# Performance work log

Measured on AMD Instinct MI355X. Metric: run time of the kernel, lower is better.

## Reference

```python
import jax, jax.numpy as jnp
import numpy as np

S = 160                 # image size (renderer default is 256; reduced for working-set budget)
SIGMA = 1.0             # soft-silhouette sharpness, in pixels
EPS = 1e-8
CHUNK = 512             # faces per rasterization chunk
ANGLE = np.pi / 2.0
VIEW_TAN = float(np.tan(np.radians(30.0)))   # nr.Renderer default viewing_angle=30
CAM_POS = np.array([0.0, 0.0, 2.732], dtype=np.float32)

# constant rotation: Rodrigues formula for axis-angle (pi/2 about y), as in nr.rotation_from_axis
_aa = ANGLE * np.array([0.0, 1.0, 0.0])
_th = np.linalg.norm(_aa)
_k = _aa / _th
_K = np.array([[0, -_k[2], _k[1]], [_k[2], 0, -_k[0]], [-_k[1], _k[0], 0]])
ROT = (np.eye(3) + np.sin(_th) * _K + (1 - np.cos(_th)) * (_K @ _K)).astype(np.float32)


def _make_uv_sphere(stacks=32, slices=64):
    verts = [[0.0, 0.0, 1.0]]
    for i in range(1, stacks):
        phi = np.pi * i / stacks
        for j in range(slices):
            th = 2 * np.pi * j / slices
            verts.append([np.sin(phi) * np.cos(th), np.sin(phi) * np.sin(th), np.cos(phi)])
    verts.append([0.0, 0.0, -1.0])
    V = len(verts)
    faces = []
    for j in range(slices):
        faces.append([0, 1 + j, 1 + (j + 1) % slices])
    for i in range(stacks - 2):
        r0 = 1 + i * slices
        r1 = r0 + slices
        for j in range(slices):
            a, b = r0 + j, r0 + (j + 1) % slices
            c, d = r1 + j, r1 + (j + 1) % slices
            faces.append([a, b, c])
            faces.append([b, d, c])
    r0 = 1 + (stacks - 2) * slices
    for j in range(slices):
        faces.append([V - 1, r0 + (j + 1) % slices, r0 + j])
    return np.asarray(verts, np.float32), np.asarray(faces, np.int32)


def setup_inputs() -> dict:
    key = jax.random.key(0)
    v, f = _make_uv_sphere()                     # V=1986, F=3968
    pad = 4096 - f.shape[0]
    f = np.concatenate([f, np.zeros((pad, 3), np.int32)], axis=0)  # degenerate pad faces
    image_ref = jax.random.uniform(key, (1, S, S), dtype=jnp.float32)
    return {"vertices": jnp.asarray(v)[None], "faces": jnp.asarray(f)[None], "image_ref": image_ref}


def _project(v):
    # world -> camera (rotate, place camera at z=2.732) -> perspective -> pixel coords
    vc = v @ ROT.T + CAM_POS                     # [V,3]
    xy = vc[:, :2] / (vc[:, 2:3] * VIEW_TAN)     # NDC in [-1,1]
    return (xy + 1.0) * (S / 2.0)                # [V,2] pixels


def _soft_coverage(pts, fv):
    # pts [P,2] pixel centers, fv [C,3,2] screen-space triangles -> coverage [P,C]
    a, b, c = fv[:, 0], fv[:, 1], fv[:, 2]

    def edge_dist(p0, p1):
        d = p1 - p0                                              # [C,2]
        cr = d[:, 0] * (pts[:, None, 1] - p0[None, :, 1]) - d[:, 1] * (pts[:, None, 0] - p0[None, :, 0])
        return cr / (jnp.sqrt(jnp.sum(d * d, -1)) + EPS)         # signed pixel distance [P,C]

    area = (b[:, 0] - a[:, 0]) * (c[:, 1] - a[:, 1]) - (b[:, 1] - a[:, 1]) * (c[:, 0] - a[:, 0])
    sg = jnp.where(area >= 0, 1.0, -1.0)[None, :]                # winding correction
    dmin = jnp.minimum(jnp.minimum(edge_dist(a, b) * sg, edge_dist(b, c) * sg), edge_dist(c, a) * sg)
    cov = jax.nn.sigmoid(dmin / SIGMA)
    return cov * (jnp.abs(area) > 1e-6)[None, :]                 # mask degenerate (padded) faces


def reference(vertices, faces, image_ref):
    v2 = _project(vertices[0])                   # [V,2]
    fv = v2[faces[0]]                            # [F,3,2]
    fvc = fv.reshape(-1, CHUNK, 3, 2)            # [F/CHUNK, CHUNK, 3, 2]
    ys, xs = jnp.meshgrid(jnp.arange(S, dtype=jnp.float32) + 0.5,
                          jnp.arange(S, dtype=jnp.float32) + 0.5, indexing="ij")
    pts = jnp.stack([xs.ravel(), ys.ravel()], -1)  # [P,2]

    cov_fn = jax.checkpoint(_soft_coverage)

    def body(not_cov, fvk):
        cov = cov_fn(pts, fvk)                   # [P,CHUNK]
        return not_cov * jnp.prod(1.0 - cov, axis=1), None

    not_cov, _ = jax.lax.scan(body, jnp.ones((S * S,), jnp.float32), fvc)
    images = (1.0 - not_cov).reshape(1, S, S)    # silhouette in [0,1]
    loss = jnp.sum((images - image_ref) ** 2)    # broadcast matches images - image_ref[None] in torch
    return images, loss
```

## Files before the change

kernel.cpp:

```cpp
#include <hip/hip_runtime.h>
#include <math.h>

#define S_IMG 160
#define NPIX (S_IMG * S_IMG)
#define NF 4096
#define NV 1986
#define TS 16
#define NTX 10
#define NTILE 100
#define CAP NF
#define SPLIT 16
#define INV_LN2 1.4426950408889634f
#define CULL_THRESH -25.0f

#define ROT_EPS 6.123234e-17f
#define CAM_Z 2.732f
#define VIEW_TAN 0.5773502691896258f

#if __has_builtin(__builtin_amdgcn_exp2f)
#define EXP2F(x) __builtin_amdgcn_exp2f(x)
#else
#define EXP2F(x) exp2f(x)
#endif

__global__ void __launch_bounds__(512) setup_cull(const float* __restrict__ verts,
                                                  const int* __restrict__ faces,
                                                  float* __restrict__ list,
                                                  int* __restrict__ nk_arr) {
    __shared__ float2 sverts[NV];
    __shared__ int wcnt[8];

    const int t = blockIdx.x;
    const int tid = threadIdx.x;
    const int wid = tid >> 6;
    const int lane = tid & 63;

    for (int i = tid; i < NV; i += 512) {
        float x = verts[3 * i], y = verts[3 * i + 1], z = verts[3 * i + 2];
        float vx = fmaf(ROT_EPS, x, z);
        float vz = fmaf(ROT_EPS, z, -x) + CAM_Z;
        float inv = __builtin_amdgcn_rcpf(vz * VIEW_TAN);
        sverts[i] = make_float2(fmaf(vx * inv, 80.0f, 80.0f),
                                fmaf(y * inv, 80.0f, 80.0f));
    }
    __syncthreads();

    const float cx = (float)((t % NTX) * TS) + 8.0f;
    const float cy = (float)((t / NTX) * TS) + 8.0f;
    float* mylist = list + (size_t)t * CAP * 12;
    int base = 0;

    for (int r = 0; r < NF / 512; ++r) {
        int f = r * 512 + tid;
        int i0 = faces[3 * f], i1 = faces[3 * f + 1], i2 = faces[3 * f + 2];
        float2 a = sverts[i0];
        float2 b = sverts[i1];
        float2 c = sverts[i2];
        float area = (b.x - a.x) * (c.y - a.y) - (b.y - a.y) * (c.x - a.x);
        float sg = (area >= 0.0f) ? INV_LN2 : -INV_LN2;
        bool valid = fabsf(area) > 1e-6f;

        float o[9];
        float umin = 1e30f;
        float2 p0s[3] = {a, b, c};
        float2 p1s[3] = {b, c, a};
#pragma unroll
        for (int e = 0; e < 3; ++e) {
            float dx = p1s[e].x - p0s[e].x;
            float dy = p1s[e].y - p0s[e].y;
            float dd = fmaf(dx, dx, dy * dy);
            float s = sg * __builtin_amdgcn_rsqf(dd);
            float A = valid ? (-dy * s) : 0.0f;
            float B = valid ? (dx * s) : 0.0f;
            float C = valid ? ((dy * p0s[e].x - dx * p0s[e].y) * s) : -1e30f;
            o[3 * e + 0] = A;
            o[3 * e + 1] = B;
            o[3 * e + 2] = C;
            float bound = fmaf(fabsf(A) + fabsf(B), 7.5f, fmaf(A, cx, fmaf(B, cy, C)));
            umin = fminf(umin, valid ? bound : -1e30f);
        }
        bool pred = umin >= CULL_THRESH;
        unsigned long long m = __ballot(pred);
        int wpop = __popcll(m);
        int prefix = __popcll(m & ((1ull << lane) - 1ull));

        __syncthreads();
        if (lane == 0) wcnt[wid] = wpop;
        __syncthreads();
        int off = base;
#pragma unroll
        for (int w = 0; w < 8; ++w) {
            int cw = wcnt[w];
            if (w < wid) off += cw;
            base += cw;
        }
        off += prefix;
        if (pred) {
            float4* dst = (float4*)(mylist + (size_t)off * 12);
            dst[0] = make_float4(o[0], o[1], o[2], o[3]);
            dst[1] = make_float4(o[4], o[5], o[6], o[7]);
            dst[2] = make_float4(o[8], 0.0f, 0.0f, 0.0f);
        }
    }
    __syncthreads();

    const int cnt = base;
    const int nkt = (cnt + 63) >> 6;
    int padcnt = nkt * 64 - cnt;
    for (int i = tid; i < padcnt; i += 512) {
        float4* dst = (float4*)(mylist + (size_t)(cnt + i) * 12);
        dst[0] = make_float4(0.0f, 0.0f, -64.0f, 0.0f);
        dst[1] = make_float4(0.0f, -64.0f, 0.0f, 0.0f);
        dst[2] = make_float4(-64.0f, 0.0f, 0.0f, 0.0f);
    }
    if (tid == 0) nk_arr[t] = nkt;
}

__global__ void __launch_bounds__(64) cover(const float* __restrict__ list,
                                            const int* __restrict__ nk_arr,
                                            float* __restrict__ pacc) {
    const int t = blockIdx.x;
    const int s = blockIdx.y;
    const int nkt = nk_arr[t];
    if (s >= nkt) return;

    const int lane = threadIdx.x;
    const int colL = lane & 15;
    const int rowL = (lane >> 4) * 4;
    const float px = (float)((t % NTX) * TS + colL) + 0.5f;
    const float py0 = (float)((t / NTX) * TS + rowL) + 0.5f;
    const float py1 = py0 + 1.0f, py2 = py0 + 2.0f, py3 = py0 + 3.0f;

    float P0 = 1.0f, P1 = 1.0f, P2 = 1.0f, P3 = 1.0f;

    for (int k = s; k < nkt; k += SPLIT) {
        const float* fptr = list + ((size_t)t * CAP + (size_t)k * 64) * 12;
#pragma unroll 4
        for (int j = 0; j < 64; ++j) {
            float4 c0 = *(const float4*)(fptr + 12 * j);
            float4 c1 = *(const float4*)(fptr + 12 * j + 4);
            float4 c2 = *(const float4*)(fptr + 12 * j + 8);
            float b1 = fmaf(c0.x, px, c0.z);
            float b2 = fmaf(c0.w, px, c1.y);
            float b3 = fmaf(c1.z, px, c2.x);
            {
                float d1 = fmaf(c0.y, py0, b1), d2 = fmaf(c1.x, py0, b2), d3 = fmaf(c1.w, py0, b3);
                float e = EXP2F(fminf(fminf(d1, d2), d3));
                P0 = fmaf(P0, e, P0);
            }
            {
                float d1 = fmaf(c0.y, py1, b1), d2 = fmaf(c1.x, py1, b2), d3 = fmaf(c1.w, py1, b3);
                float e = EXP2F(fminf(fminf(d1, d2), d3));
                P1 = fmaf(P1, e, P1);
            }
            {
                float d1 = fmaf(c0.y, py2, b1), d2 = fmaf(c1.x, py2, b2), d3 = fmaf(c1.w, py2, b3);
                float e = EXP2F(fminf(fminf(d1, d2), d3));
                P2 = fmaf(P2, e, P2);
            }
            {
                float d1 = fmaf(c0.y, py3, b1), d2 = fmaf(c1.x, py3, b2), d3 = fmaf(c1.w, py3, b3);
                float e = EXP2F(fminf(fminf(d1, d2), d3));
                P3 = fmaf(P3, e, P3);
            }
        }
    }

    size_t base = ((size_t)t * SPLIT + s) * 256 + (size_t)rowL * 16 + colL;
    pacc[base] = __builtin_amdgcn_rcpf(P0);
    pacc[base + 16] = __builtin_amdgcn_rcpf(P1);
    pacc[base + 32] = __builtin_amdgcn_rcpf(P2);
    pacc[base + 48] = __builtin_amdgcn_rcpf(P3);
}

__global__ void __launch_bounds__(256) finish(const float* __restrict__ pacc,
                                              const int* __restrict__ nk_arr,
                                              const float* __restrict__ img_ref,
                                              float* __restrict__ out,
                                              float* __restrict__ bsums) {
    const int t = blockIdx.x;
    const int tid = threadIdx.x;
    const int ns = min(nk_arr[t], SPLIT);
    float prod = 1.0f;
    for (int sI = 0; sI < ns; ++sI) prod *= pacc[((size_t)t * SPLIT + sI) * 256 + tid];
    float img = 1.0f - prod;
    int col = (t % NTX) * TS + (tid & 15);
    int row = (t / NTX) * TS + (tid >> 4);
    int p = row * S_IMG + col;
    out[p] = img;
    float d = img - img_ref[p];
    float sq = d * d;
#pragma unroll
    for (int off = 32; off > 0; off >>= 1) sq += __shfl_down(sq, off);
    __shared__ float red[4];
    int lane = tid & 63;
    int wid = tid >> 6;
    if (lane == 0) red[wid] = sq;
    __syncthreads();
    if (tid == 0) bsums[t] = (red[0] + red[1]) + (red[2] + red[3]);
}

__global__ void __launch_bounds__(64) loss_kernel(const float* __restrict__ bsums,
                                                  float* __restrict__ loss_out) {
    int lane = threadIdx.x;
    float v = 0.0f;
    if (lane < NTILE) v = bsums[lane];
    if (lane + 64 < NTILE) v += bsums[lane + 64];
#pragma unroll
    for (int off = 32; off > 0; off >>= 1) v += __shfl_down(v, off);
    if (lane == 0) loss_out[0] = v;
}

extern "C" void kernel_launch(void* const* d_in, const int* in_sizes, int n_in,
                              void* d_out, int out_size, void* d_ws, size_t ws_size,
                              hipStream_t stream) {
    const float* verts = (const float*)d_in[0];
    const int* faces = (const int*)d_in[1];
    const float* img_ref = (const float*)d_in[2];
    float* out = (float*)d_out;

    float* list = (float*)d_ws;
    float* pacc = list + (size_t)NTILE * CAP * 12;
    int* nk_arr = (int*)(pacc + (size_t)NTILE * SPLIT * 256);
    float* bsums = (float*)(nk_arr + 128);

    setup_cull<<<NTILE, 512, 0, stream>>>(verts, faces, list, nk_arr);
    cover<<<dim3(NTILE, SPLIT), 64, 0, stream>>>(list, nk_arr, pacc);
    finish<<<NTILE, 256, 0, stream>>>(pacc, nk_arr, img_ref, out, bsums);
    loss_kernel<<<1, 64, 0, stream>>>(bsums, out + NPIX);
}
```

Measured before the change: 39.35 us.

## Flatten tile×chunk work into a compacted item list with LDS-staged face data

```diff
diff --git a/kernel.cpp b/kernel.cpp
--- a/kernel.cpp
+++ b/kernel.cpp
@@ -9,7 +9,8 @@
 #define NTX 10
 #define NTILE 100
 #define CAP NF
-#define SPLIT 16
+#define MAXK 64
+#define NBLK 512
 #define INV_LN2 1.4426950408889634f
 #define CULL_THRESH -25.0f
 
@@ -116,30 +117,55 @@
     if (tid == 0) nk_arr[t] = nkt;
 }
 
-__global__ void __launch_bounds__(64) cover(const float* __restrict__ list,
-                                            const int* __restrict__ nk_arr,
-                                            float* __restrict__ pacc) {
-    const int t = blockIdx.x;
-    const int s = blockIdx.y;
-    const int nkt = nk_arr[t];
-    if (s >= nkt) return;
-
-    const int lane = threadIdx.x;
-    const int colL = lane & 15;
-    const int rowL = (lane >> 4) * 4;
-    const float px = (float)((t % NTX) * TS + colL) + 0.5f;
-    const float py0 = (float)((t / NTX) * TS + rowL) + 0.5f;
-    const float py1 = py0 + 1.0f, py2 = py0 + 2.0f, py3 = py0 + 3.0f;
-
-    float P0 = 1.0f, P1 = 1.0f, P2 = 1.0f, P3 = 1.0f;
-
-    for (int k = s; k < nkt; k += SPLIT) {
-        const float* fptr = list + ((size_t)t * CAP + (size_t)k * 64) * 12;
-#pragma unroll 4
+__global__ void __launch_bounds__(128) build_items(const int* __restrict__ nk_arr,
+                                                   int* __restrict__ cumk,
+                                                   int* __restrict__ items) {
+    __shared__ int scum[NTILE + 1];
+    if (threadIdx.x == 0) {
+        int acc = 0;
+        for (int t = 0; t < NTILE; ++t) { scum[t] = acc; acc += nk_arr[t]; }
+        scum[NTILE] = acc;
+        cumk[NTILE] = acc;
+    }
+    __syncthreads();
+    for (int t = threadIdx.x; t < NTILE; t += 128) {
+        int b = scum[t], n = scum[t + 1] - b;
+        cumk[t] = b;
+        for (int k = 0; k < n; ++k) items[b + k] = (t << 8) | k;
+    }
+}
+
+__global__ void __launch_bounds__(256) cover(const float* __restrict__ list,
+                                             const int* __restrict__ cumk,
+                                             const int* __restrict__ items,
+                                             float* __restrict__ partials) {
+    __shared__ float4 slot[4][64 * 3];
+    const int wid = threadIdx.x >> 6;
+    const int lane = threadIdx.x & 63;
+    const int NIT = cumk[NTILE];
+    const int NW = NBLK * 4;
+    float4* myslot = slot[wid];
+
+    for (int p = blockIdx.x * 4 + wid; p < NIT; p += NW) {
+        int item = items[p];
+        int t = item >> 8, k = item & 255;
+
+        const float4* src = (const float4*)(list + ((size_t)t * CAP + (size_t)k * 64) * 12);
+#pragma unroll
+        for (int i = 0; i < 3; ++i) myslot[lane + i * 64] = src[lane + i * 64];
+        asm volatile("s_waitcnt lgkmcnt(0)" ::: "memory");
+
+        const int colL = lane & 15;
+        const int rowL = (lane >> 4) * 4;
+        const float px = (float)((t % NTX) * TS + colL) + 0.5f;
+        const float py0 = (float)((t / NTX) * TS + rowL) + 0.5f;
+        const float py1 = py0 + 1.0f, py2 = py0 + 2.0f, py3 = py0 + 3.0f;
+
+        float P0 = 1.0f, P1 = 1.0f, P2 = 1.0f, P3 = 1.0f;
         for (int j = 0; j < 64; ++j) {
-            float4 c0 = *(const float4*)(fptr + 12 * j);
-            float4 c1 = *(const float4*)(fptr + 12 * j + 4);
-            float4 c2 = *(const float4*)(fptr + 12 * j + 8);
+            float4 c0 = myslot[3 * j];
+            float4 c1 = myslot[3 * j + 1];
+            float4 c2 = myslot[3 * j + 2];
             float b1 = fmaf(c0.x, px, c0.z);
             float b2 = fmaf(c0.w, px, c1.y);
             float b3 = fmaf(c1.z, px, c2.x);
@@ -164,25 +190,26 @@
                 P3 = fmaf(P3, e, P3);
             }
         }
-    }
-
-    size_t base = ((size_t)t * SPLIT + s) * 256 + (size_t)rowL * 16 + colL;
-    pacc[base] = __builtin_amdgcn_rcpf(P0);
-    pacc[base + 16] = __builtin_amdgcn_rcpf(P1);
-    pacc[base + 32] = __builtin_amdgcn_rcpf(P2);
-    pacc[base + 48] = __builtin_amdgcn_rcpf(P3);
-}
-
-__global__ void __launch_bounds__(256) finish(const float* __restrict__ pacc,
+        asm volatile("" ::: "memory");
+
+        size_t base = ((size_t)t * MAXK + k) * 256 + (size_t)rowL * 16 + colL;
+        partials[base] = __builtin_amdgcn_rcpf(P0);
+        partials[base + 16] = __builtin_amdgcn_rcpf(P1);
+        partials[base + 32] = __builtin_amdgcn_rcpf(P2);
+        partials[base + 48] = __builtin_amdgcn_rcpf(P3);
+    }
+}
+
+__global__ void __launch_bounds__(256) finish(const float* __restrict__ partials,
                                               const int* __restrict__ nk_arr,
                                               const float* __restrict__ img_ref,
                                               float* __restrict__ out,
                                               float* __restrict__ bsums) {
     const int t = blockIdx.x;
     const int tid = threadIdx.x;
-    const int ns = min(nk_arr[t], SPLIT);
+    const int nkt = nk_arr[t];
     float prod = 1.0f;
-    for (int sI = 0; sI < ns; ++sI) prod *= pacc[((size_t)t * SPLIT + sI) * 256 + tid];
+    for (int k = 0; k < nkt; ++k) prod *= partials[((size_t)t * MAXK + k) * 256 + tid];
     float img = 1.0f - prod;
     int col = (t % NTX) * TS + (tid & 15);
     int row = (t / NTX) * TS + (tid >> 4);
@@ -220,12 +247,15 @@
     float* out = (float*)d_out;
 
     float* list = (float*)d_ws;
-    float* pacc = list + (size_t)NTILE * CAP * 12;
-    int* nk_arr = (int*)(pacc + (size_t)NTILE * SPLIT * 256);
-    float* bsums = (float*)(nk_arr + 128);
+    float* partials = list + (size_t)NTILE * CAP * 12;
+    int* nk_arr = (int*)(partials + (size_t)NTILE * MAXK * 256);
+    int* cumk = nk_arr + 128;
+    int* items = cumk + 128;
+    float* bsums = (float*)(items + NTILE * MAXK + 128);
 
     setup_cull<<<NTILE, 512, 0, stream>>>(verts, faces, list, nk_arr);
-    cover<<<dim3(NTILE, SPLIT), 64, 0, stream>>>(list, nk_arr, pacc);
-    finish<<<NTILE, 256, 0, stream>>>(pacc, nk_arr, img_ref, out, bsums);
+    build_items<<<1, 128, 0, stream>>>(nk_arr, cumk, items);
+    cover<<<NBLK, 256, 0, stream>>>(list, cumk, items, partials);
+    finish<<<NTILE, 256, 0, stream>>>(partials, nk_arr, img_ref, out, bsums);
     loss_kernel<<<1, 64, 0, stream>>>(bsums, out + NPIX);
 }
```

Result: no change. 38.73 us (-1.6%).

## Use 16x32 tiles, one wave per face chunk with LDS-staged coefficients

Applied to the files above, without the earlier changes.

```diff
diff --git a/kernel.cpp b/kernel.cpp
--- a/kernel.cpp
+++ b/kernel.cpp
@@ -5,11 +5,11 @@
 #define NPIX (S_IMG * S_IMG)
 #define NF 4096
 #define NV 1986
-#define TS 16
-#define NTX 10
-#define NTILE 100
+#define NTTX 10
+#define NTILE2 50
 #define CAP NF
-#define SPLIT 16
+#define MAXK 64
+#define NBLK3 800
 #define INV_LN2 1.4426950408889634f
 #define CULL_THRESH -25.0f
 
@@ -23,19 +23,20 @@
 #define EXP2F(x) exp2f(x)
 #endif
 
-__global__ void __launch_bounds__(512) setup_cull(const float* __restrict__ verts,
-                                                  const int* __restrict__ faces,
-                                                  float* __restrict__ list,
-                                                  int* __restrict__ nk_arr) {
+__global__ void __launch_bounds__(1024) setup_cull(const float* __restrict__ verts,
+                                                   const int* __restrict__ faces,
+                                                   float4* __restrict__ qlist,
+                                                   float* __restrict__ c3list,
+                                                   int* __restrict__ nk_arr) {
     __shared__ float2 sverts[NV];
-    __shared__ int wcnt[8];
+    __shared__ int wcnt[16];
 
     const int t = blockIdx.x;
     const int tid = threadIdx.x;
     const int wid = tid >> 6;
     const int lane = tid & 63;
 
-    for (int i = tid; i < NV; i += 512) {
+    for (int i = tid; i < NV; i += 1024) {
         float x = verts[3 * i], y = verts[3 * i + 1], z = verts[3 * i + 2];
         float vx = fmaf(ROT_EPS, x, z);
         float vz = fmaf(ROT_EPS, z, -x) + CAM_Z;
@@ -45,13 +46,14 @@
     }
     __syncthreads();
 
-    const float cx = (float)((t % NTX) * TS) + 8.0f;
-    const float cy = (float)((t / NTX) * TS) + 8.0f;
-    float* mylist = list + (size_t)t * CAP * 12;
+    const float cx = (float)((t % NTTX) * 16) + 8.0f;
+    const float cy = (float)((t / NTTX) * 32) + 16.0f;
+    float4* myq = qlist + (size_t)t * CAP * 2;
+    float* myc = c3list + (size_t)t * CAP;
     int base = 0;
 
-    for (int r = 0; r < NF / 512; ++r) {
-        int f = r * 512 + tid;
+    for (int r = 0; r < NF / 1024; ++r) {
+        int f = r * 1024 + tid;
         int i0 = faces[3 * f], i1 = faces[3 * f + 1], i2 = faces[3 * f + 2];
         float2 a = sverts[i0];
         float2 b = sverts[i1];
@@ -76,7 +78,8 @@
             o[3 * e + 0] = A;
             o[3 * e + 1] = B;
             o[3 * e + 2] = C;
-            float bound = fmaf(fabsf(A) + fabsf(B), 7.5f, fmaf(A, cx, fmaf(B, cy, C)));
+            float bound = fmaf(fabsf(A), 7.5f,
+                         fmaf(fabsf(B), 15.5f, fmaf(A, cx, fmaf(B, cy, C))));
             umin = fminf(umin, valid ? bound : -1e30f);
         }
         bool pred = umin >= CULL_THRESH;
@@ -89,17 +92,16 @@
         __syncthreads();
         int off = base;
 #pragma unroll
-        for (int w = 0; w < 8; ++w) {
+        for (int w = 0; w < 16; ++w) {
             int cw = wcnt[w];
             if (w < wid) off += cw;
             base += cw;
         }
         off += prefix;
         if (pred) {
-            float4* dst = (float4*)(mylist + (size_t)off * 12);
-            dst[0] = make_float4(o[0], o[1], o[2], o[3]);
-            dst[1] = make_float4(o[4], o[5], o[6], o[7]);
-            dst[2] = make_float4(o[8], 0.0f, 0.0f, 0.0f);
+            myq[(size_t)off * 2] = make_float4(o[0], o[1], o[2], o[3]);
+            myq[(size_t)off * 2 + 1] = make_float4(o[4], o[5], o[6], o[7]);
+            myc[off] = o[8];
         }
     }
     __syncthreads();
@@ -107,105 +109,111 @@
     const int cnt = base;
     const int nkt = (cnt + 63) >> 6;
     int padcnt = nkt * 64 - cnt;
-    for (int i = tid; i < padcnt; i += 512) {
-        float4* dst = (float4*)(mylist + (size_t)(cnt + i) * 12);
-        dst[0] = make_float4(0.0f, 0.0f, -64.0f, 0.0f);
-        dst[1] = make_float4(0.0f, -64.0f, 0.0f, 0.0f);
-        dst[2] = make_float4(-64.0f, 0.0f, 0.0f, 0.0f);
+    for (int i = tid; i < padcnt; i += 1024) {
+        myq[(size_t)(cnt + i) * 2] = make_float4(0.0f, 0.0f, -64.0f, 0.0f);
+        myq[(size_t)(cnt + i) * 2 + 1] = make_float4(0.0f, -64.0f, 0.0f, 0.0f);
+        myc[cnt + i] = -64.0f;
     }
     if (tid == 0) nk_arr[t] = nkt;
 }
 
-__global__ void __launch_bounds__(64) cover(const float* __restrict__ list,
-                                            const int* __restrict__ nk_arr,
-                                            float* __restrict__ pacc) {
-    const int t = blockIdx.x;
-    const int s = blockIdx.y;
-    const int nkt = nk_arr[t];
-    if (s >= nkt) return;
-
-    const int lane = threadIdx.x;
+__global__ void __launch_bounds__(256) cover(const float4* __restrict__ qlist,
+                                             const float* __restrict__ c3list,
+                                             const int* __restrict__ nk_arr,
+                                             float* __restrict__ partials) {
+    __shared__ float4 sq[4][128];
+    __shared__ float sc[4][64];
+    const int wid = threadIdx.x >> 6;
+    const int lane = threadIdx.x & 63;
+    const int p = blockIdx.x * 4 + wid;
+    const int t = p >> 6;
+    const int k = p & 63;
+    if (k >= nk_arr[t]) return;
+
+    {
+        const float4* srcq = qlist + ((size_t)t * CAP + (size_t)k * 64) * 2;
+        const float* srcc = c3list + (size_t)t * CAP + (size_t)k * 64;
+        sq[wid][lane * 2] = srcq[lane * 2];
+        sq[wid][lane * 2 + 1] = srcq[lane * 2 + 1];
+        sc[wid][lane] = srcc[lane];
+    }
+    asm volatile("s_waitcnt lgkmcnt(0)" ::: "memory");
+
     const int colL = lane & 15;
-    const int rowL = (lane >> 4) * 4;
-    const float px = (float)((t % NTX) * TS + colL) + 0.5f;
-    const float py0 = (float)((t / NTX) * TS + rowL) + 0.5f;
-    const float py1 = py0 + 1.0f, py2 = py0 + 2.0f, py3 = py0 + 3.0f;
+    const int rowB = (lane >> 4) * 8;
+    const float px = (float)((t % NTTX) * 16 + colL) + 0.5f;
+    const float py0 = (float)((t / NTTX) * 32 + rowB) + 0.5f;
 
     float P0 = 1.0f, P1 = 1.0f, P2 = 1.0f, P3 = 1.0f;
-
-    for (int k = s; k < nkt; k += SPLIT) {
-        const float* fptr = list + ((size_t)t * CAP + (size_t)k * 64) * 12;
-#pragma unroll 4
-        for (int j = 0; j < 64; ++j) {
-            float4 c0 = *(const float4*)(fptr + 12 * j);
-            float4 c1 = *(const float4*)(fptr + 12 * j + 4);
-            float4 c2 = *(const float4*)(fptr + 12 * j + 8);
-            float b1 = fmaf(c0.x, px, c0.z);
-            float b2 = fmaf(c0.w, px, c1.y);
-            float b3 = fmaf(c1.z, px, c2.x);
-            {
-                float d1 = fmaf(c0.y, py0, b1), d2 = fmaf(c1.x, py0, b2), d3 = fmaf(c1.w, py0, b3);
-                float e = EXP2F(fminf(fminf(d1, d2), d3));
-                P0 = fmaf(P0, e, P0);
-            }
-            {
-                float d1 = fmaf(c0.y, py1, b1), d2 = fmaf(c1.x, py1, b2), d3 = fmaf(c1.w, py1, b3);
-                float e = EXP2F(fminf(fminf(d1, d2), d3));
-                P1 = fmaf(P1, e, P1);
-            }
-            {
-                float d1 = fmaf(c0.y, py2, b1), d2 = fmaf(c1.x, py2, b2), d3 = fmaf(c1.w, py2, b3);
-                float e = EXP2F(fminf(fminf(d1, d2), d3));
-                P2 = fmaf(P2, e, P2);
-            }
-            {
-                float d1 = fmaf(c0.y, py3, b1), d2 = fmaf(c1.x, py3, b2), d3 = fmaf(c1.w, py3, b3);
-                float e = EXP2F(fminf(fminf(d1, d2), d3));
-                P3 = fmaf(P3, e, P3);
-            }
-        }
-    }
-
-    size_t base = ((size_t)t * SPLIT + s) * 256 + (size_t)rowL * 16 + colL;
-    pacc[base] = __builtin_amdgcn_rcpf(P0);
-    pacc[base + 16] = __builtin_amdgcn_rcpf(P1);
-    pacc[base + 32] = __builtin_amdgcn_rcpf(P2);
-    pacc[base + 48] = __builtin_amdgcn_rcpf(P3);
-}
-
-__global__ void __launch_bounds__(256) finish(const float* __restrict__ pacc,
+    float P4 = 1.0f, P5 = 1.0f, P6 = 1.0f, P7 = 1.0f;
+
+    for (int j = 0; j < 64; ++j) {
+        float4 q0 = sq[wid][2 * j];
+        float4 q1 = sq[wid][2 * j + 1];
+        float c3 = sc[wid][j];
+        float b1 = fmaf(q0.x, px, q0.z);
+        float b2 = fmaf(q0.w, px, q1.y);
+        float b3 = fmaf(q1.z, px, c3);
+#define ROW(rr, PP)                                                            \
+        {                                                                      \
+            float py = py0 + (float)(rr);                                      \
+            float d1 = fmaf(q0.y, py, b1);                                     \
+            float d2 = fmaf(q1.x, py, b2);                                     \
+            float d3 = fmaf(q1.w, py, b3);                                     \
+            float e = EXP2F(fminf(fminf(d1, d2), d3));                         \
+            PP = fmaf(PP, e, PP);                                              \
+        }
+        ROW(0, P0) ROW(1, P1) ROW(2, P2) ROW(3, P3)
+        ROW(4, P4) ROW(5, P5) ROW(6, P6) ROW(7, P7)
+#undef ROW
+    }
+
+    size_t base = ((size_t)t * MAXK + k) * 512 + (size_t)rowB * 16 + colL;
+    partials[base] = __builtin_amdgcn_rcpf(P0);
+    partials[base + 16] = __builtin_amdgcn_rcpf(P1);
+    partials[base + 32] = __builtin_amdgcn_rcpf(P2);
+    partials[base + 48] = __builtin_amdgcn_rcpf(P3);
+    partials[base + 64] = __builtin_amdgcn_rcpf(P4);
+    partials[base + 80] = __builtin_amdgcn_rcpf(P5);
+    partials[base + 96] = __builtin_amdgcn_rcpf(P6);
+    partials[base + 112] = __builtin_amdgcn_rcpf(P7);
+}
+
+__global__ void __launch_bounds__(512) finish(const float* __restrict__ partials,
                                               const int* __restrict__ nk_arr,
                                               const float* __restrict__ img_ref,
                                               float* __restrict__ out,
                                               float* __restrict__ bsums) {
     const int t = blockIdx.x;
     const int tid = threadIdx.x;
-    const int ns = min(nk_arr[t], SPLIT);
+    const int nkt = nk_arr[t];
     float prod = 1.0f;
-    for (int sI = 0; sI < ns; ++sI) prod *= pacc[((size_t)t * SPLIT + sI) * 256 + tid];
+#pragma unroll 4
+    for (int k = 0; k < nkt; ++k) prod *= partials[((size_t)t * MAXK + k) * 512 + tid];
     float img = 1.0f - prod;
-    int col = (t % NTX) * TS + (tid & 15);
-    int row = (t / NTX) * TS + (tid >> 4);
+    int col = (t % NTTX) * 16 + (tid & 15);
+    int row = (t / NTTX) * 32 + (tid >> 4);
     int p = row * S_IMG + col;
     out[p] = img;
     float d = img - img_ref[p];
     float sq = d * d;
 #pragma unroll
     for (int off = 32; off > 0; off >>= 1) sq += __shfl_down(sq, off);
-    __shared__ float red[4];
+    __shared__ float red[8];
     int lane = tid & 63;
     int wid = tid >> 6;
     if (lane == 0) red[wid] = sq;
     __syncthreads();
-    if (tid == 0) bsums[t] = (red[0] + red[1]) + (red[2] + red[3]);
+    if (tid == 0)
+        bsums[t] = ((red[0] + red[1]) + (red[2] + red[3])) +
+                   ((red[4] + red[5]) + (red[6] + red[7]));
 }
 
 __global__ void __launch_bounds__(64) loss_kernel(const float* __restrict__ bsums,
                                                   float* __restrict__ loss_out) {
     int lane = threadIdx.x;
     float v = 0.0f;
-    if (lane < NTILE) v = bsums[lane];
-    if (lane + 64 < NTILE) v += bsums[lane + 64];
+    if (lane < NTILE2) v = bsums[lane];
 #pragma unroll
     for (int off = 32; off > 0; off >>= 1) v += __shfl_down(v, off);
     if (lane == 0) loss_out[0] = v;
@@ -219,13 +227,14 @@
     const float* img_ref = (const float*)d_in[2];
     float* out = (float*)d_out;
 
-    float* list = (float*)d_ws;
-    float* pacc = list + (size_t)NTILE * CAP * 12;
-    int* nk_arr = (int*)(pacc + (size_t)NTILE * SPLIT * 256);
+    float4* qlist = (float4*)d_ws;
+    float* c3list = (float*)(qlist + (size_t)NTILE2 * CAP * 2);
+    float* partials = c3list + (size_t)NTILE2 * CAP;
+    int* nk_arr = (int*)(partials + (size_t)NTILE2 * MAXK * 512);
     float* bsums = (float*)(nk_arr + 128);
 
-    setup_cull<<<NTILE, 512, 0, stream>>>(verts, faces, list, nk_arr);
-    cover<<<dim3(NTILE, SPLIT), 64, 0, stream>>>(list, nk_arr, pacc);
-    finish<<<NTILE, 256, 0, stream>>>(pacc, nk_arr, img_ref, out, bsums);
+    setup_cull<<<NTILE2, 1024, 0, stream>>>(verts, faces, qlist, c3list, nk_arr);
+    cover<<<NBLK3, 256, 0, stream>>>(qlist, c3list, nk_arr, partials);
+    finish<<<NTILE2, 512, 0, stream>>>(partials, nk_arr, img_ref, out, bsums);
     loss_kernel<<<1, 64, 0, stream>>>(bsums, out + NPIX);
 }
```

Result: slower. 44.88 us (+14.1%).
